# Performance work log

Measured on AMD Instinct MI355X. Metric: run time of the kernel, lower is better.

The kernel has to match this reference:

```python
import jax, jax.numpy as jnp
import numpy as np

# Config matching init_kwargs: dim=256, input_resolution=(64,64), num_heads=8,
# stride=2, dynamic_factor=2, window_size=8, Attention_Group=2, postype='rel', k=None
DIM, H, W = 256, 64, 64
HEADS, HG, STRIDE, WS, FACTOR = 8, 2, 2, 8, 2.0
GC = DIM // HG                 # channels per attention group (offset net width)
HC = DIM // HEADS              # per-head channels
RH, RW = H // STRIDE, W // STRIDE
WH, WW = H // WS, W // WS
B = 2
MLP_HID = 4 * DIM
EPS = 1e-5


def _grid_sample(img, grid):
    # img: (N, C, H, W); grid: (N, Hg, Wg, 2) with (row, col) in [-1, 1].
    # Bilinear, align_corners=True, zero padding (matches F.grid_sample).
    N, C, Hi, Wi = img.shape
    rows = (grid[..., 0] + 1.0) * 0.5 * (Hi - 1)
    cols = (grid[..., 1] + 1.0) * 0.5 * (Wi - 1)
    r0f = jnp.floor(rows); c0f = jnp.floor(cols)
    wr = rows - r0f; wc = cols - c0f
    r0 = r0f.astype(jnp.int32); c0 = c0f.astype(jnp.int32)

    def gather(ri, ci):
        valid = ((ri >= 0) & (ri < Hi) & (ci >= 0) & (ci < Wi)).astype(img.dtype)
        rc = jnp.clip(ri, 0, Hi - 1); cc = jnp.clip(ci, 0, Wi - 1)
        vals = jax.vmap(lambda im, r, c: im[:, r, c])(img, rc, cc)  # (N, C, Hg, Wg)
        return vals * valid[:, None]

    return (gather(r0, c0) * ((1 - wr) * (1 - wc))[:, None]
            + gather(r0, c0 + 1) * ((1 - wr) * wc)[:, None]
            + gather(r0 + 1, c0) * (wr * (1 - wc))[:, None]
            + gather(r0 + 1, c0 + 1) * (wr * wc)[:, None])


def _ln2d(z, g, b):
    mu = jnp.mean(z, axis=1, keepdims=True)
    var = jnp.var(z, axis=1, keepdims=True)
    return (z - mu) * jax.lax.rsqrt(var + EPS) * g[None, :, None, None] + b[None, :, None, None]


def _conv1x1(z, w, b=None):
    out = jnp.einsum('oc,bchw->bohw', w, z)
    return out if b is None else out + b[None, :, None, None]


def _forward(x, ln1_g, ln1_b, q_w, q_b, k_w, k_b, v_w, v_b,
             off1_w, off2_w, off3_w, bn_g, bn_b, bn_m, bn_v, off4_w,
             posembed, proj_w, proj_b, ln2_g, ln2_b,
             mlp_w1, mlp_b1, mlp_w2, mlp_b2):
    Bx, C = x.shape[0], x.shape[1]
    R, NW, WT = RH * RW, WH * WW, WS * WS
    scale = C ** -0.5  # original uses dim**-0.5 (not head_dim) as default qk scale

    xa = _ln2d(x, ln1_g, ln1_b)
    q = _conv1x1(xa, q_w, q_b)

    # ---- per-group offset prediction: 3 depthwise strided convs -> BN -> GELU -> 1x1 ----
    qg = q.reshape(Bx * HG, GC, H, W)

    def dw(z, w):
        return jax.lax.conv_general_dilated(z, w, (2, 2), ((1, 1), (1, 1)),
                feature_group_count=GC, dimension_numbers=('NCHW', 'OIHW', 'NCHW'))

    o = dw(dw(dw(qg, off1_w), off2_w), off3_w)  # (B*HG, GC, WH, WW)
    o = (o - bn_m[None, :, None, None]) * jax.lax.rsqrt(bn_v + EPS)[None, :, None, None]
    o = o * bn_g[None, :, None, None] + bn_b[None, :, None, None]
    o = jax.nn.gelu(o, approximate=False)
    off = jnp.einsum('oc,bchw->bohw', off4_w, o)               # (B*HG, 2R, WH, WW)
    off = off.reshape(Bx * HG, 2, R, NW).transpose(0, 3, 2, 1)  # (B*HG, NW, R, 2)
    ranges = jnp.array([1.0 / H, 1.0 / W], dtype=x.dtype)
    off = jnp.tanh(off) * ranges * FACTOR

    # ---- reference points normalized to [-1, 1] (align_corners=True convention) ----
    ref_r = (jnp.arange(RH, dtype=x.dtype) * STRIDE) / (H - 1) * 2.0 - 1.0
    ref_c = (jnp.arange(RW, dtype=x.dtype) * STRIDE) / (W - 1) * 2.0 - 1.0
    ref = jnp.stack(jnp.meshgrid(ref_r, ref_c, indexing='ij'), axis=-1).reshape(R, 2)
    grid = off + ref[None, None]                                # (B*HG, NW, R, 2)

    # ---- deformable gather of values at predicted sample locations ----
    value = xa.reshape(Bx * HG, GC, H, W)
    samp = _grid_sample(value, grid).reshape(Bx, C, NW, R)

    kk = _conv1x1(samp, k_w, k_b).reshape(Bx * HEADS, HC, NW, R).transpose(0, 2, 1, 3)
    vv = _conv1x1(samp, v_w, v_b).reshape(Bx * HEADS, HC, NW, R).transpose(0, 2, 1, 3)

    # ---- windowed queries ----
    wq = q.reshape(Bx * HEADS, HC, H, W).transpose(0, 2, 3, 1)
    wq = wq.reshape(Bx * HEADS, WH, WS, WW, WS, HC).transpose(0, 1, 3, 2, 4, 5)
    wq = wq.reshape(Bx * HEADS, NW, WT, HC) * scale

    attn = jnp.einsum('nwqc,nwcr->nwqr', wq, kk)                # (B*h, NW, WT, R)

    # ---- relative position bias: query pixel vs. (stride-spaced) reference point ----
    rel_y = (jnp.arange(RH) * STRIDE)[None, :] - jnp.arange(H)[:, None] + (H - 1)  # (H, RH)
    rel_x = (jnp.arange(RW) * STRIDE)[None, :] - jnp.arange(W)[:, None] + (W - 1)  # (W, RW)
    t = posembed[:, rel_y, :]                                   # (h, H, RH, 2W-1)
    bias = t[:, :, :, rel_x]                                    # (h, H, RH, W, RW)
    bias = bias.transpose(0, 1, 3, 2, 4).reshape(HEADS, H, W, R)
    bias = bias.reshape(HEADS, WH, WS, WW, WS, R).transpose(0, 1, 3, 2, 4, 5)
    bias = bias.reshape(HEADS, NW, WT, R)

    attn = attn.reshape(Bx, HEADS, NW, WT, R) + bias[None]
    attn = jax.nn.softmax(attn, axis=-1).reshape(Bx * HEADS, NW, WT, R)
    out = jnp.einsum('nwqr,nwcr->nwqc', attn, vv)               # (B*h, NW, WT, HC)
    out = out.reshape(Bx * HEADS, WH, WW, WS, WS, HC).transpose(0, 1, 3, 2, 4, 5)
    out = out.reshape(Bx, HEADS, H, W, HC).transpose(0, 1, 4, 2, 3).reshape(Bx, C, H, W)
    out = _conv1x1(out, proj_w, proj_b)

    x = x + out
    xm = _ln2d(x, ln2_g, ln2_b)
    hdn = jax.nn.gelu(_conv1x1(xm, mlp_w1, mlp_b1), approximate=False)
    return x + _conv1x1(hdn, mlp_w2, mlp_b2)


def setup_inputs() -> dict:
    key = jax.random.key(0)
    ks = jax.random.split(key, 16)
    f32 = jnp.float32

    def n(k, shape, std=0.02):
        return jax.random.normal(k, shape, dtype=f32) * std

    R = RH * RW
    return {
        'x': jax.random.normal(ks[0], (B, DIM, H, W), dtype=f32),
        'ln1_g': jnp.ones((DIM,), f32), 'ln1_b': jnp.zeros((DIM,), f32),
        'q_w': n(ks[1], (DIM, DIM)), 'q_b': jnp.zeros((DIM,), f32),
        'k_w': n(ks[2], (DIM, DIM)), 'k_b': jnp.zeros((DIM,), f32),
        'v_w': n(ks[3], (DIM, DIM)), 'v_b': jnp.zeros((DIM,), f32),
        'off1_w': n(ks[4], (GC, 1, 3, 3)),
        'off2_w': n(ks[5], (GC, 1, 3, 3)),
        'off3_w': n(ks[6], (GC, 1, 3, 3)),
        'bn_g': jnp.ones((GC,), f32), 'bn_b': jnp.zeros((GC,), f32),
        'bn_m': jnp.zeros((GC,), f32), 'bn_v': jnp.ones((GC,), f32),
        'off4_w': n(ks[7], (2 * R, GC)),
        'posembed': n(ks[8], (HEADS, 2 * H - 1, 2 * W - 1), std=0.01),
        'proj_w': n(ks[9], (DIM, DIM)), 'proj_b': jnp.zeros((DIM,), f32),
        'ln2_g': jnp.ones((DIM,), f32), 'ln2_b': jnp.zeros((DIM,), f32),
        'mlp_w1': n(ks[10], (MLP_HID, DIM)), 'mlp_b1': jnp.zeros((MLP_HID,), f32),
        'mlp_w2': n(ks[11], (DIM, MLP_HID)), 'mlp_b2': jnp.zeros((DIM,), f32),
    }


def reference(x, ln1_g, ln1_b, q_w, q_b, k_w, k_b, v_w, v_b,
              off1_w, off2_w, off3_w, bn_g, bn_b, bn_m, bn_v, off4_w,
              posembed, proj_w, proj_b, ln2_g, ln2_b,
              mlp_w1, mlp_b1, mlp_w2, mlp_b2):
    return _forward(x, ln1_g, ln1_b, q_w, q_b, k_w, k_b, v_w, v_b,
                    off1_w, off2_w, off3_w, bn_g, bn_b, bn_m, bn_v, off4_w,
                    posembed, proj_w, proj_b, ln2_g, ln2_b,
                    mlp_w1, mlp_b1, mlp_w2, mlp_b2)
```

## Files before the change

kernel.cpp:

```cpp
#include <hip/hip_runtime.h>
#include <hip/hip_bf16.h>
#include <math.h>


typedef __hip_bfloat16 bf16;
typedef __bf16 bf16x8 __attribute__((ext_vector_type(8)));
typedef float f32x4 __attribute__((ext_vector_type(4)));
typedef unsigned int u32x4 __attribute__((ext_vector_type(4)));

union U16x8 { uint4 u4; u32x4 v4; unsigned short us[8]; };

__device__ __forceinline__ float cvt(float x) { return x; }
__device__ __forceinline__ float cvt(bf16 x) { return __bfloat162float(x); }
__device__ __forceinline__ float b2f(unsigned short u) {
  union { float f; unsigned int v; } x; x.v = ((unsigned int)u) << 16; return x.f;
}
__device__ __forceinline__ unsigned short f2b(float f) {
  bf16 h = __float2bfloat16(f);
  return *reinterpret_cast<unsigned short*>(&h);
}
__device__ __forceinline__ float gelu_f(float x) {
  return 0.5f * x * (1.0f + erff(x * 0.7071067811865475f));
}
__device__ __forceinline__ void stout(float* p, float v) { *p = v; }
__device__ __forceinline__ void stout(bf16* p, float v) { *p = __float2bfloat16(v); }

__global__ __launch_bounds__(256) void setup_kernel(
    const float* __restrict__ x, const float* __restrict__ g,
    const float* __restrict__ bta,
    const float* __restrict__ q_w, const float* __restrict__ q_b,
    const float* __restrict__ k_w, const float* __restrict__ v_w,
    const float* __restrict__ pjw, const float* __restrict__ w1,
    const float* __restrict__ w2, const float* __restrict__ off4w,
    bf16* __restrict__ out, float* __restrict__ xnhwc,
    unsigned short* __restrict__ wqkv, float* __restrict__ bqkv,
    unsigned short* __restrict__ wproj, unsigned short* __restrict__ wmlp1,
    unsigned short* __restrict__ wmlp2, unsigned short* __restrict__ woff4i)
{
  __shared__ float s1[8][32], s2[8][32];
  __shared__ unsigned short tb[32][264];
  int bid = blockIdx.x;
  int t = threadIdx.x;
  if (bid < 256) {
    int pos = t & 31, cs = t >> 5;
    int p = bid * 32 + pos;
    int bb = p >> 12, hw = p & 4095;
    const float* xp = x + (size_t)bb * 256 * 4096 + hw;
    float vloc[32];
    float sum = 0.f, ss = 0.f;
#pragma unroll
    for (int i = 0; i < 32; ++i) {
      float v = xp[(size_t)(cs * 32 + i) * 4096];
      vloc[i] = v; sum += v; ss += v * v;
    }
    s1[cs][pos] = sum; s2[cs][pos] = ss;
    {
      float* xo = xnhwc + (size_t)p * 256 + cs * 32;
#pragma unroll
      for (int qd = 0; qd < 8; ++qd)
        *(float4*)(xo + qd * 4) = make_float4(vloc[qd*4], vloc[qd*4+1],
                                              vloc[qd*4+2], vloc[qd*4+3]);
    }
    __syncthreads();
    if (cs == 0) {
      float S = 0.f, Q = 0.f;
#pragma unroll
      for (int i = 0; i < 8; ++i) { S += s1[i][pos]; Q += s2[i][pos]; }
      float mu = S * (1.f / 256.f);
      float var = Q * (1.f / 256.f) - mu * mu;
      s1[0][pos] = mu;
      s2[0][pos] = rsqrtf(var + 1e-5f);
    }
    __syncthreads();
    float mu = s1[0][pos], rs = s2[0][pos];
#pragma unroll
    for (int i = 0; i < 32; ++i) {
      int c = cs * 32 + i;
      tb[pos][c] = f2b((vloc[i] - mu) * rs * g[c] + bta[c]);
    }
    __syncthreads();
    int px = t >> 3, grp = t & 7;
    bf16* op = out + ((size_t)bid * 32 + px) * 256 + grp * 32;
#pragma unroll
    for (int q = 0; q < 4; ++q)
      *(uint4*)(op + q * 8) = *(const uint4*)&tb[px][grp * 32 + q * 8];
  } else {
    int idx = (bid - 256) * 256 + t;
    const int S0 = 768 * 256;
    const int S1 = S0 + 768;
    const int S2 = S1 + 256 * 256;
    const int S3 = S2 + 1024 * 256;
    const int S4 = S3 + 256 * 1024;
    const int S5 = S4 + 2048 * 128;
    if (idx < S0) {
      int n = idx >> 8, c = idx & 255;
      float v;
      if (n < 256)       v = q_w[n * 256 + c];
      else if (n < 512)  v = k_w[(n - 256) * 256 + c];
      else               v = v_w[(n - 512) * 256 + c];
      wqkv[idx] = f2b(v);
    } else if (idx < S1) {
      int n = idx - S0;
      bqkv[n] = (n < 256) ? q_b[n] : 0.f;
    } else if (idx < S2) {
      wproj[idx - S1] = f2b(pjw[idx - S1]);
    } else if (idx < S3) {
      wmlp1[idx - S2] = f2b(w1[idx - S2]);
    } else if (idx < S4) {
      wmlp2[idx - S3] = f2b(w2[idx - S3]);
    } else if (idx < S5) {
      int kk = idx - S4;
      int n = kk >> 7, c = kk & 127;
      woff4i[kk] = f2b(off4w[((size_t)((n & 1) * 1024 + (n >> 1))) * 128 + c]);
    }
  }
}

__global__ __launch_bounds__(256) void ln2_kernel(
    const bf16* __restrict__ xin, const float* __restrict__ g,
    const float* __restrict__ bta, bf16* __restrict__ out)
{
  __shared__ float sa[8][32], sb[8][32];
  __shared__ float mu_s[32], rs_s[32];
  int t = threadIdx.x;
  int px = t >> 3, grp = t & 7;
  size_t p = (size_t)blockIdx.x * 32 + px;
  const bf16* xp = xin + p * 256 + grp * 32;
  float v[32]; float sum = 0.f, ss = 0.f;
#pragma unroll
  for (int q = 0; q < 4; ++q) {
    U16x8 u; u.u4 = *(const uint4*)(xp + q * 8);
#pragma unroll
    for (int j = 0; j < 8; ++j) {
      float f = b2f(u.us[j]); v[q * 8 + j] = f; sum += f; ss += f * f;
    }
  }
  sa[grp][px] = sum; sb[grp][px] = ss;
  __syncthreads();
  if (t < 32) {
    float S = 0.f, Q = 0.f;
#pragma unroll
    for (int i = 0; i < 8; ++i) { S += sa[i][t]; Q += sb[i][t]; }
    float mu = S * (1.f / 256.f);
    mu_s[t] = mu;
    rs_s[t] = rsqrtf(Q * (1.f / 256.f) - mu * mu + 1e-5f);
  }
  __syncthreads();
  float mu = mu_s[px], rs = rs_s[px];
  bf16* op = out + p * 256 + grp * 32;
#pragma unroll
  for (int q = 0; q < 4; ++q) {
    U16x8 o;
#pragma unroll
    for (int j = 0; j < 8; ++j) {
      int c = grp * 32 + q * 8 + j;
      o.us[j] = f2b((v[q * 8 + j] - mu) * rs * g[c] + bta[c]);
    }
    *(uint4*)(op + q * 8) = o.u4;
  }
}

template<int OUTM, int RESM, int ACT, int BM>
__global__ __launch_bounds__(256) void mgemm_kernel(
    const bf16* __restrict__ A, const unsigned short* __restrict__ Bw,
    const float* __restrict__ bias, const void* __restrict__ res,
    void* __restrict__ out, int N, int K, int lda, int ldb)
{
  constexpr int MT = BM / 32;
  constexpr int AB_BYTES = (BM + 64) * 72 * 2;
  constexpr int T_LD = BM + 5;
  constexpr int T_BYTES = 64 * T_LD * 4;
  constexpr int SH_BYTES = (OUTM == 1 && T_BYTES > AB_BYTES) ? T_BYTES : AB_BYTES;
  __shared__ __attribute__((aligned(16))) char shraw[SH_BYTES];
  auto As = reinterpret_cast<unsigned short(*)[72]>(shraw);
  auto Bs = reinterpret_cast<unsigned short(*)[72]>(shraw + BM * 72 * 2);
  float (*T)[T_LD] = reinterpret_cast<float(*)[T_LD]>(shraw);

  int t = threadIdx.x;
  int m0 = blockIdx.y * BM, n0 = blockIdx.x * 64;
  int lane = t & 63, w = t >> 6;
  int l15 = lane & 15, quad = lane >> 4;
  int wm = (w >> 1) * (BM / 2), wn = (w & 1) * 32;
  f32x4 acc[MT][2];
#pragma unroll
  for (int mt = 0; mt < MT; ++mt)
#pragma unroll
    for (int nt = 0; nt < 2; ++nt) acc[mt][nt] = (f32x4){0.f, 0.f, 0.f, 0.f};

  for (int k0 = 0; k0 < K; k0 += 64) {
#pragma unroll
    for (int i = 0; i < MT; ++i) {
      int idx = t + i * 256;
      int m = idx >> 3, oc = (idx & 7) * 8;
      *(uint4*)&As[m][oc] = *(const uint4*)(A + (size_t)(m0 + m) * lda + k0 + oc);
    }
#pragma unroll
    for (int i = 0; i < 2; ++i) {
      int idx = t + i * 256;
      int n = idx >> 3, oc = (idx & 7) * 8;
      *(uint4*)&Bs[n][oc] = *(const uint4*)(Bw + (size_t)(n0 + n) * ldb + k0 + oc);
    }
    __syncthreads();
#pragma unroll
    for (int ks = 0; ks < 2; ++ks) {
      bf16x8 af[MT], bfr[2];
#pragma unroll
      for (int mt = 0; mt < MT; ++mt)
        af[mt] = __builtin_bit_cast(bf16x8,
            *(const uint4*)&As[wm + mt * 16 + l15][ks * 32 + quad * 8]);
#pragma unroll
      for (int nt = 0; nt < 2; ++nt)
        bfr[nt] = __builtin_bit_cast(bf16x8,
            *(const uint4*)&Bs[wn + nt * 16 + l15][ks * 32 + quad * 8]);
#pragma unroll
      for (int mt = 0; mt < MT; ++mt)
#pragma unroll
        for (int nt = 0; nt < 2; ++nt)
          acc[mt][nt] = __builtin_amdgcn_mfma_f32_16x16x32_bf16(
              af[mt], bfr[nt], acc[mt][nt], 0, 0, 0);
    }
    __syncthreads();
  }
  float bv[2];
#pragma unroll
  for (int nt = 0; nt < 2; ++nt)
    bv[nt] = bias ? bias[n0 + wn + nt * 16 + l15] : 0.f;
#pragma unroll
  for (int mt = 0; mt < MT; ++mt) {
#pragma unroll
    for (int nt = 0; nt < 2; ++nt) {
#pragma unroll
      for (int reg = 0; reg < 4; ++reg) {
        int m = m0 + wm + mt * 16 + quad * 4 + reg;
        int n = n0 + wn + nt * 16 + l15;
        float v = acc[mt][nt][reg] + bv[nt];
        if constexpr (ACT == 1) v = gelu_f(v);
        if constexpr (RESM == 1)
          v += ((const float*)res)[(size_t)m * N + n];
        if constexpr (RESM == 2)
          v += b2f(((const unsigned short*)res)[(size_t)m * N + n]);
        if constexpr (OUTM == 0)
          ((unsigned short*)out)[(size_t)m * N + n] = f2b(v);
        if constexpr (OUTM == 1)
          T[(n - n0)][(m - m0)] = v;
        if constexpr (OUTM == 4)
          ((unsigned short*)out)[((size_t)(n >> 8) * 8192 + m) * 256 + (n & 255)] = f2b(v);
        if constexpr (OUTM == 5) {
          float val = tanhf(v) * (2.0f / 64.0f);
          int r = n >> 1, coord = n & 1;
          int rc = coord ? (r & 31) : (r >> 5);
          float ref = rc * (4.0f / 63.0f) - 1.0f;
          float pix = (val + ref + 1.0f) * 31.5f;
          float other = __shfl_xor(pix, 1, 64);
          if (coord == 0) {
            float rowp = pix, colp = other;
            float r0f = floorf(rowp), c0f = floorf(colp);
            float wr = rowp - r0f, wc = colp - c0f;
            int r0 = (int)r0f, c0 = (int)c0f;
            bool rv0 = ((unsigned)r0 < 64u), rv1 = ((unsigned)(r0 + 1) < 64u);
            bool cv0 = ((unsigned)c0 < 64u), cv1 = ((unsigned)(c0 + 1) < 64u);
            float4 w4;
            w4.x = (rv0 && cv0) ? (1.f - wr) * (1.f - wc) : 0.f;
            w4.y = (rv0 && cv1) ? (1.f - wr) * wc : 0.f;
            w4.z = (rv1 && cv0) ? wr * (1.f - wc) : 0.f;
            w4.w = (rv1 && cv1) ? wr * wc : 0.f;
            ((int*)out)[(size_t)m * 1024 + r] = r0 * 64 + c0;
            *(float4*)((float*)res + ((size_t)m * 1024 + r) * 4) = w4;
          }
        }
      }
    }
  }
  if constexpr (OUTM == 1) {
    __syncthreads();
    constexpr int SEGS = BM / 32;
    int units = 64 * SEGS;
    if (t < units) {
      int nl = t / SEGS, seg = t % SEGS;
      int bI = m0 >> 12, hw0 = m0 & 4095;
      float* op = (float*)out + ((size_t)bI * 256 + n0 + nl) * 4096 + hw0 + seg * 32;
#pragma unroll
      for (int k = 0; k < 32; ++k) op[k] = T[nl][seg * 32 + k];
    }
  }
}

template<typename TI, typename TO, int IC>
__global__ __launch_bounds__(256) void dwconv_kernel(
    const TI* __restrict__ in, const float* __restrict__ wgt,
    TO* __restrict__ out, int Hi, int Wi, int Ho, int Wo, int fuse,
    const float* __restrict__ bg_, const float* __restrict__ bb_,
    const float* __restrict__ bm_, const float* __restrict__ bv_)
{
  int idx = blockIdx.x * 256 + threadIdx.x;
  int c = idx & 127;
  int pp = idx >> 7;
  int ow = pp % Wo, oh = (pp / Wo) % Ho, bgi = pp / (Wo * Ho);
  const TI* ip;
  if constexpr (IC == 256)
    ip = in + ((size_t)(bgi >> 1) * 4096) * 256 + (bgi & 1) * 128 + c;
  else
    ip = in + ((size_t)bgi * Hi * Wi) * 128 + c;
  float acc = 0.f;
#pragma unroll
  for (int ky = 0; ky < 3; ++ky) {
    int ih = oh * 2 - 1 + ky;
    if ((unsigned)ih >= (unsigned)Hi) continue;
#pragma unroll
    for (int kx = 0; kx < 3; ++kx) {
      int iw = ow * 2 - 1 + kx;
      if ((unsigned)iw >= (unsigned)Wi) continue;
      acc += wgt[c * 9 + ky * 3 + kx] * cvt(ip[(size_t)(ih * Wi + iw) * IC]);
    }
  }
  if (fuse) {
    acc = (acc - bm_[c]) * rsqrtf(bv_[c] + 1e-5f) * bg_[c] + bb_[c];
    acc = gelu_f(acc);
  }
  stout(out + idx, acc);
}

__global__ __launch_bounds__(256) void gather1_kernel(
    const unsigned short* __restrict__ img,
    const int* __restrict__ goff, const float* __restrict__ gwt,
    unsigned short* __restrict__ outp)
{
  int blk = blockIdx.x;
  blk = (blk & 7) * 2048 + (blk >> 3);
  int t = threadIdx.x;
  int pos = blk * 8 + (t >> 5);
  int oct = t & 31;
  int r = pos & 1023;
  int nw = (pos >> 10) & 63;
  int b = pos >> 16;
  int ch0 = oct * 8;
  int g = oct >> 4;

  size_t cbase = ((size_t)(b * 2 + g) * 64 + nw) * 1024 + r;
  int base = goff[cbase];
  f32x4 wv = *(const f32x4*)(gwt + cbase * 4);
  int o00 = min(max(base, 0), 4095);
  int o01 = min(max(base + 1, 0), 4095);
  int o10 = min(max(base + 64, 0), 4095);
  int o11 = min(max(base + 65, 0), 4095);
  size_t pb = ((size_t)b * 4096) * 256 + ch0;
  uint4 cc[4];
  cc[0] = *(const uint4*)(img + pb + (size_t)o00 * 256);
  cc[1] = *(const uint4*)(img + pb + (size_t)o01 * 256);
  cc[2] = *(const uint4*)(img + pb + (size_t)o10 * 256);
  cc[3] = *(const uint4*)(img + pb + (size_t)o11 * 256);

  float a[8] = {0.f, 0.f, 0.f, 0.f, 0.f, 0.f, 0.f, 0.f};
#pragma unroll
  for (int c4 = 0; c4 < 4; ++c4) {
    U16x8 u; u.u4 = cc[c4];
    float wvv = wv[c4];
#pragma unroll
    for (int j = 0; j < 8; ++j) a[j] += wvv * b2f(u.us[j]);
  }
  U16x8 o;
#pragma unroll
  for (int j = 0; j < 8; ++j) o.us[j] = f2b(a[j]);
  int head = oct >> 2, chh = (oct & 3) * 8;
  size_t obase = (((size_t)(b * 8 + head) * 64 + nw) * 1024 + r) * 32 + chh;
  __builtin_nontemporal_store(o.v4, (u32x4*)(outp + obase));
}

__global__ __launch_bounds__(256) void attn2_kernel(
    const bf16* __restrict__ qbuf, const unsigned short* __restrict__ Ks,
    const unsigned short* __restrict__ Vs, const float* __restrict__ vbv,
    const float* __restrict__ pe, bf16* __restrict__ aout)
{
  __shared__ unsigned short vs[2][32][72];
  __shared__ unsigned short PsQs[64][72];
  __shared__ unsigned short pesb[70][72];

  int blk = blockIdx.x;
  int b = blk & 1, head = (blk >> 1) & 7, nw = blk >> 4;
  int wh = nw >> 3, ww = nw & 7;
  int t = threadIdx.x;
  int lane = t & 63, w = t >> 6;
  int l15 = lane & 15, quad = lane >> 4;
  int qc0 = head * 32;
  int vr = t >> 2, vseg = t & 3;

  size_t kvbase = ((size_t)(b * 8 + head) * 64 + nw) * 1024 * 32;
  const unsigned short* Kb = Ks + kvbase;
  const unsigned short* Vb = Vs + kvbase;

  {
    int qt = t >> 2, oct = t & 3;
    int h = wh * 8 + (qt >> 3), wcol = ww * 8 + (qt & 7);
    const bf16* src = qbuf + ((size_t)b * 4096 + h * 64 + wcol) * 256 + qc0 + oct * 8;
    U16x8 u; u.u4 = *(const uint4*)src;
    U16x8 o;
#pragma unroll
    for (int j = 0; j < 8; ++j) o.us[j] = f2b(b2f(u.us[j]) * 0.0625f);
    *(uint4*)&PsQs[qt][oct * 8] = o.u4;
  }
  int ry0 = 56 - wh * 8, rx0 = 56 - ww * 8;
  for (int i = t; i < 70 * 70; i += 256) {
    int yy = i / 70, xx = i % 70;
    pesb[yy][xx] = f2b(pe[(size_t)head * 16129 + (ry0 + yy) * 127 + rx0 + xx]);
  }
  {
    U16x8 vu; vu.u4 = *(const uint4*)(Vb + (size_t)t * 8);
#pragma unroll
    for (int j = 0; j < 8; ++j) {
      int row = vseg * 8 + j;
      vs[0][row][vr ^ (((row >> 3) & 3) * 8)] = vu.us[j];
    }
  }
  uint4 kf[4];
#pragma unroll
  for (int nt = 0; nt < 4; ++nt)
    kf[nt] = *(const uint4*)(Kb + (size_t)(nt * 16 + l15) * 32 + quad * 8);
  __syncthreads();

  bf16x8 aQ = __builtin_bit_cast(bf16x8, *(const uint4*)&PsQs[w * 16 + l15][quad * 8]);
  float l[4] = {0.f, 0.f, 0.f, 0.f};
  f32x4 oacc[2];
  oacc[0] = (f32x4){0.f, 0.f, 0.f, 0.f};
  oacc[1] = (f32x4){0.f, 0.f, 0.f, 0.f};

  uint4 vcn = make_uint4(0u, 0u, 0u, 0u);
  uint4 kfn[4];
  for (int c = 0; c < 16; ++c) {
    int cur = c & 1, rc0 = c * 64;
    if (c) {
      U16x8 vu; vu.u4 = vcn;
#pragma unroll
      for (int j = 0; j < 8; ++j) {
        int row = vseg * 8 + j;
        vs[cur][row][vr ^ (((row >> 3) & 3) * 8)] = vu.us[j];
      }
      __syncthreads();
    }
    if (c < 15) {
      size_t nb = (size_t)(rc0 + 64) * 32;
      vcn = *(const uint4*)(Vb + nb + (size_t)t * 8);
#pragma unroll
      for (int nt = 0; nt < 4; ++nt)
        kfn[nt] = *(const uint4*)(Kb + nb + (size_t)(nt * 16 + l15) * 32 + quad * 8);
    }

    f32x4 s[4];
#pragma unroll
    for (int nt = 0; nt < 4; ++nt) {
      bf16x8 bK = __builtin_bit_cast(bf16x8, kf[nt]);
      f32x4 z = (f32x4){0.f, 0.f, 0.f, 0.f};
      s[nt] = __builtin_amdgcn_mfma_f32_16x16x32_bf16(aQ, bK, z, 0, 0, 0);
    }
#pragma unroll
    for (int nt = 0; nt < 4; ++nt) {
      int rg_ = nt * 16 + l15;
      int rrow = (rc0 + rg_) >> 5, rcol = rg_ & 31;
#pragma unroll
      for (int reg = 0; reg < 4; ++reg) {
        int q = w * 16 + quad * 4 + reg;
        s[nt][reg] += b2f(pesb[2 * rrow + 7 - (q >> 3)][2 * rcol + 7 - (q & 7)]);
      }
    }
#pragma unroll
    for (int reg = 0; reg < 4; ++reg) {
      float ps = 0.f;
#pragma unroll
      for (int nt = 0; nt < 4; ++nt) {
        float p = __expf(s[nt][reg]);
        PsQs[w * 16 + quad * 4 + reg][nt * 16 + l15] = f2b(p);
        ps += p;
      }
      l[reg] += ps;
    }
#pragma unroll
    for (int kst = 0; kst < 2; ++kst) {
      uint4 up = *(const uint4*)&PsQs[w * 16 + l15][kst * 32 + quad * 8];
      bf16x8 pA = __builtin_bit_cast(bf16x8, up);
#pragma unroll
      for (int nt2 = 0; nt2 < 2; ++nt2) {
        int row = nt2 * 16 + l15;
        int cbase = (kst * 32 + quad * 8) ^ (((row >> 3) & 3) * 8);
        uint4 uv = *(const uint4*)&vs[cur][row][cbase];
        bf16x8 vB = __builtin_bit_cast(bf16x8, uv);
        oacc[nt2] = __builtin_amdgcn_mfma_f32_16x16x32_bf16(pA, vB, oacc[nt2], 0, 0, 0);
      }
    }
    if (c < 15) {
#pragma unroll
      for (int nt = 0; nt < 4; ++nt) kf[nt] = kfn[nt];
    }
  }
#pragma unroll
  for (int reg = 0; reg < 4; ++reg) {
    l[reg] += __shfl_xor(l[reg], 1, 64);
    l[reg] += __shfl_xor(l[reg], 2, 64);
    l[reg] += __shfl_xor(l[reg], 4, 64);
    l[reg] += __shfl_xor(l[reg], 8, 64);
  }
#pragma unroll
  for (int nt2 = 0; nt2 < 2; ++nt2) {
    float vbias = vbv[qc0 + nt2 * 16 + l15];
#pragma unroll
    for (int reg = 0; reg < 4; ++reg) {
      int q = w * 16 + quad * 4 + reg;
      size_t p = (size_t)b * 4096 + (wh * 8 + (q >> 3)) * 64 + ww * 8 + (q & 7);
      aout[p * 256 + qc0 + nt2 * 16 + l15] =
          __float2bfloat16(oacc[nt2][reg] / l[reg] + vbias);
    }
  }
}

extern "C" void kernel_launch(void* const* d_in, const int* in_sizes, int n_in,
                              void* d_out, int out_size, void* d_ws, size_t ws_size,
                              hipStream_t stream) {
  (void)in_sizes; (void)n_in; (void)out_size; (void)ws_size;
  const float* x     = (const float*)d_in[0];
  const float* ln1g  = (const float*)d_in[1];
  const float* ln1b  = (const float*)d_in[2];
  const float* q_w   = (const float*)d_in[3];
  const float* q_b   = (const float*)d_in[4];
  const float* k_w   = (const float*)d_in[5];
  const float* k_b   = (const float*)d_in[6];
  const float* v_w   = (const float*)d_in[7];
  const float* v_b   = (const float*)d_in[8];
  const float* off1w = (const float*)d_in[9];
  const float* off2w = (const float*)d_in[10];
  const float* off3w = (const float*)d_in[11];
  const float* bng   = (const float*)d_in[12];
  const float* bnb   = (const float*)d_in[13];
  const float* bnm   = (const float*)d_in[14];
  const float* bnv   = (const float*)d_in[15];
  const float* off4w = (const float*)d_in[16];
  const float* pe    = (const float*)d_in[17];
  const float* pjw   = (const float*)d_in[18];
  const float* pjb   = (const float*)d_in[19];
  const float* ln2g  = (const float*)d_in[20];
  const float* ln2b  = (const float*)d_in[21];
  const float* w1    = (const float*)d_in[22];
  const float* b1    = (const float*)d_in[23];
  const float* w2    = (const float*)d_in[24];
  const float* b2    = (const float*)d_in[25];
  (void)k_b;
  float* outp = (float*)d_out;

  char* W = (char*)d_ws;
  bf16*  xa    = (bf16*) (W + 0);
  float* dw1   = (float*)(W + 8388608);
  float* dw2   = (float*)(W + 10485760);
  bf16*  dw3b  = (bf16*) (W + 11010048);
  bf16*  qkv   = (bf16*) (W + 13238272);
  bf16*  qb    = qkv;
  bf16*  Kimg  = qkv + 2097152;
  bf16*  Vimg  = qkv + 2 * 2097152;
  bf16*  x2    = (bf16*) (W + 34209792);
  float* xnhwc = (float*)(W + 38404096);
  unsigned short* wqkv   = (unsigned short*)(W + 46792704);
  float*          bqkv   = (float*)         (W + 47448064);
  unsigned short* wproj  = (unsigned short*)(W + 47453184);
  unsigned short* wmlp1  = (unsigned short*)(W + 47584256);
  unsigned short* wmlp2  = (unsigned short*)(W + 48108544);
  unsigned short* woff4i = (unsigned short*)(W + 48632832);
  int*   goff  = (int*)  (W + 49157120);
  float* gwt   = (float*)(W + 50205696);
  unsigned short* Ksmp = (unsigned short*)(W + 54525952);
  unsigned short* Vsmp = (unsigned short*)(W + 121634816);
  bf16*  aout = xa;
  bf16*  xm   = xa;
  bf16*  hdn  = Kimg;

  setup_kernel<<<4356, 256, 0, stream>>>(
      x, ln1g, ln1b, q_w, q_b, k_w, v_w, pjw, w1, w2, off4w,
      xa, xnhwc, wqkv, bqkv, wproj, wmlp1, wmlp2, woff4i);
  mgemm_kernel<4, 0, 0, 128><<<dim3(12, 64), 256, 0, stream>>>(
      xa, wqkv, bqkv, nullptr, qkv, 768, 256, 256, 256);
  dwconv_kernel<bf16, float, 256><<<2048, 256, 0, stream>>>(
      qb, off1w, dw1, 64, 64, 32, 32, 0, nullptr, nullptr, nullptr, nullptr);
  dwconv_kernel<float, float, 128><<<512, 256, 0, stream>>>(
      dw1, off2w, dw2, 32, 32, 16, 16, 0, nullptr, nullptr, nullptr, nullptr);
  dwconv_kernel<float, bf16, 128><<<128, 256, 0, stream>>>(
      dw2, off3w, dw3b, 16, 16, 8, 8, 1, bng, bnb, bnm, bnv);
  mgemm_kernel<5, 0, 0, 128><<<dim3(32, 2), 256, 0, stream>>>(
      dw3b, woff4i, nullptr, (const void*)gwt, goff, 2048, 128, 128, 128);
  gather1_kernel<<<16384, 256, 0, stream>>>(
      (const unsigned short*)Kimg, goff, gwt, Ksmp);
  gather1_kernel<<<16384, 256, 0, stream>>>(
      (const unsigned short*)Vimg, goff, gwt, Vsmp);
  attn2_kernel<<<1024, 256, 0, stream>>>(
      qb, Ksmp, Vsmp, v_b, pe, aout);
  mgemm_kernel<0, 1, 0, 64><<<dim3(4, 128), 256, 0, stream>>>(
      aout, wproj, pjb, (const void*)xnhwc, x2, 256, 256, 256, 256);
  ln2_kernel<<<256, 256, 0, stream>>>(x2, ln2g, ln2b, xm);
  mgemm_kernel<0, 0, 1, 128><<<dim3(16, 64), 256, 0, stream>>>(
      xm, wmlp1, b1, nullptr, hdn, 1024, 256, 256, 256);
  mgemm_kernel<1, 2, 0, 64><<<dim3(4, 128), 256, 0, stream>>>(
      hdn, wmlp2, b2, (const void*)x2, outp, 256, 1024, 1024, 1024);
}
```

Baseline: 283.6 us.

## Gather V transposed and feed attention MFMA directly from registers

A new gather kernel writes sampled V in a channel-major (transposed) layout, so the attention kernel can load V B-operands straight from global memory into registers. This removes the per-chunk LDS transpose and its __syncthreads. The softmax also moves to exp2 by folding log2(e) into the Q scale and the position-embedding table. The positional-bias lookup is simplified to two 32-bit LDS reads per tile. In exchange, each thread in the gather kernel holds more registers (an 8x8 accumulator), and the V global loads in attention are strided by 1024 elements.

```diff
diff --git a/kernel.cpp b/kernel.cpp
--- a/kernel.cpp
+++ b/kernel.cpp
@@ -9,11 +9,18 @@
 typedef unsigned int u32x4 __attribute__((ext_vector_type(4)));
 
 union U16x8 { uint4 u4; u32x4 v4; unsigned short us[8]; };
+union FU { float f; unsigned int u; };
 
 __device__ __forceinline__ float cvt(float x) { return x; }
 __device__ __forceinline__ float cvt(bf16 x) { return __bfloat162float(x); }
 __device__ __forceinline__ float b2f(unsigned short u) {
   union { float f; unsigned int v; } x; x.v = ((unsigned int)u) << 16; return x.f;
+}
+__device__ __forceinline__ float hi2f(unsigned int u) {
+  FU x; x.u = u & 0xffff0000u; return x.f;
+}
+__device__ __forceinline__ float lo2f(unsigned int u) {
+  FU x; x.u = u << 16; return x.f;
 }
 __device__ __forceinline__ unsigned short f2b(float f) {
   bf16 h = __float2bfloat16(f);
@@ -366,15 +373,75 @@
   __builtin_nontemporal_store(o.v4, (u32x4*)(outp + obase));
 }
 
-__global__ __launch_bounds__(256) void attn2_kernel(
+__global__ __launch_bounds__(256) void gathert_kernel(
+    const unsigned short* __restrict__ img,
+    const int* __restrict__ goff, const float* __restrict__ gwt,
+    unsigned short* __restrict__ outp)
+{
+  int t = threadIdx.x;
+  int l = t & 63, wv_ = t >> 6;
+  int gw = blockIdx.x * 4 + wv_;
+  int win = gw >> 6;
+  int wq = gw & 63;
+  int ocb = wq & 3;
+  int r0 = (wq >> 2) * 64;
+  int b = win >> 6, nw = win & 63;
+  int lo3 = l & 7, hi3 = l >> 3;
+  int oc = ocb * 8 + hi3;
+  int ch0 = oc * 8;
+  int g = oc >> 4;
+  int rl = r0 + lo3 * 8;
+
+  size_t cb0 = ((size_t)(b * 2 + g) * 64 + nw) * 1024 + rl;
+  size_t pb = (size_t)b * 4096 * 256 + ch0;
+
+  float acc[8][8];
+#pragma unroll
+  for (int j = 0; j < 8; ++j)
+#pragma unroll
+    for (int i = 0; i < 8; ++i) acc[j][i] = 0.f;
+
+#pragma unroll
+  for (int i = 0; i < 8; ++i) {
+    int base = goff[cb0 + i];
+    f32x4 wv4 = *(const f32x4*)(gwt + (cb0 + i) * 4);
+    int o00 = min(max(base, 0), 4095);
+    int o01 = min(max(base + 1, 0), 4095);
+    int o10 = min(max(base + 64, 0), 4095);
+    int o11 = min(max(base + 65, 0), 4095);
+    uint4 cc[4];
+    cc[0] = *(const uint4*)(img + pb + (size_t)o00 * 256);
+    cc[1] = *(const uint4*)(img + pb + (size_t)o01 * 256);
+    cc[2] = *(const uint4*)(img + pb + (size_t)o10 * 256);
+    cc[3] = *(const uint4*)(img + pb + (size_t)o11 * 256);
+#pragma unroll
+    for (int c4 = 0; c4 < 4; ++c4) {
+      U16x8 u; u.u4 = cc[c4];
+      float wvv = wv4[c4];
+#pragma unroll
+      for (int j = 0; j < 8; ++j) acc[j][i] += wvv * b2f(u.us[j]);
+    }
+  }
+  int head = oc >> 2;
+  size_t rowb0 = (((size_t)(b * 8 + head) * 64 + nw) * 32 + (oc & 3) * 8);
+#pragma unroll
+  for (int j = 0; j < 8; ++j) {
+    U16x8 o;
+#pragma unroll
+    for (int k = 0; k < 8; ++k) o.us[k] = f2b(acc[j][k]);
+    __builtin_nontemporal_store(o.v4, (u32x4*)(outp + (rowb0 + j) * 1024 + rl));
+  }
+}
+
+__global__ __launch_bounds__(256) void attn3_kernel(
     const bf16* __restrict__ qbuf, const unsigned short* __restrict__ Ks,
-    const unsigned short* __restrict__ Vs, const float* __restrict__ vbv,
+    const unsigned short* __restrict__ Vts, const float* __restrict__ vbv,
     const float* __restrict__ pe, bf16* __restrict__ aout)
 {
-  __shared__ unsigned short vs[2][32][72];
   __shared__ unsigned short PsQs[64][72];
   __shared__ unsigned short pesb[70][72];
 
+  const float LOG2E = 1.4426950408889634f;
   int blk = blockIdx.x;
   int b = blk & 1, head = (blk >> 1) & 7, nw = blk >> 4;
   int wh = nw >> 3, ww = nw & 7;
@@ -382,11 +449,10 @@
   int lane = t & 63, w = t >> 6;
   int l15 = lane & 15, quad = lane >> 4;
   int qc0 = head * 32;
-  int vr = t >> 2, vseg = t & 3;
-
-  size_t kvbase = ((size_t)(b * 8 + head) * 64 + nw) * 1024 * 32;
+
+  size_t kvbase = ((size_t)(b * 8 + head) * 64 + nw) * 32768;
   const unsigned short* Kb = Ks + kvbase;
-  const unsigned short* Vb = Vs + kvbase;
+  const unsigned short* Vt = Vts + kvbase;
 
   {
     int qt = t >> 2, oct = t & 3;
@@ -395,26 +461,24 @@
     U16x8 u; u.u4 = *(const uint4*)src;
     U16x8 o;
 #pragma unroll
-    for (int j = 0; j < 8; ++j) o.us[j] = f2b(b2f(u.us[j]) * 0.0625f);
+    for (int j = 0; j < 8; ++j) o.us[j] = f2b(b2f(u.us[j]) * (0.0625f * LOG2E));
     *(uint4*)&PsQs[qt][oct * 8] = o.u4;
   }
   int ry0 = 56 - wh * 8, rx0 = 56 - ww * 8;
   for (int i = t; i < 70 * 70; i += 256) {
     int yy = i / 70, xx = i % 70;
-    pesb[yy][xx] = f2b(pe[(size_t)head * 16129 + (ry0 + yy) * 127 + rx0 + xx]);
-  }
-  {
-    U16x8 vu; vu.u4 = *(const uint4*)(Vb + (size_t)t * 8);
-#pragma unroll
-    for (int j = 0; j < 8; ++j) {
-      int row = vseg * 8 + j;
-      vs[0][row][vr ^ (((row >> 3) & 3) * 8)] = vu.us[j];
-    }
-  }
-  uint4 kf[4];
+    pesb[yy][xx] = f2b(pe[(size_t)head * 16129 + (ry0 + yy) * 127 + rx0 + xx] * LOG2E);
+  }
+  uint4 kf[4], vf[4];
 #pragma unroll
   for (int nt = 0; nt < 4; ++nt)
     kf[nt] = *(const uint4*)(Kb + (size_t)(nt * 16 + l15) * 32 + quad * 8);
+#pragma unroll
+  for (int kst = 0; kst < 2; ++kst)
+#pragma unroll
+    for (int nt2 = 0; nt2 < 2; ++nt2)
+      vf[kst * 2 + nt2] = *(const uint4*)(Vt + (size_t)(nt2 * 16 + l15) * 1024 +
+                                          kst * 32 + quad * 8);
   __syncthreads();
 
   bf16x8 aQ = __builtin_bit_cast(bf16x8, *(const uint4*)&PsQs[w * 16 + l15][quad * 8]);
@@ -423,25 +487,23 @@
   oacc[0] = (f32x4){0.f, 0.f, 0.f, 0.f};
   oacc[1] = (f32x4){0.f, 0.f, 0.f, 0.f};
 
-  uint4 vcn = make_uint4(0u, 0u, 0u, 0u);
-  uint4 kfn[4];
+  int rowbase = 7 - (w * 2 + (quad >> 1));
+  int Cb = 2 * l15 + 7 - (quad & 1) * 4;
+
+  uint4 kfn[4], vfn[4];
   for (int c = 0; c < 16; ++c) {
-    int cur = c & 1, rc0 = c * 64;
-    if (c) {
-      U16x8 vu; vu.u4 = vcn;
-#pragma unroll
-      for (int j = 0; j < 8; ++j) {
-        int row = vseg * 8 + j;
-        vs[cur][row][vr ^ (((row >> 3) & 3) * 8)] = vu.us[j];
-      }
-      __syncthreads();
-    }
+    int rc0 = c * 64;
     if (c < 15) {
-      size_t nb = (size_t)(rc0 + 64) * 32;
-      vcn = *(const uint4*)(Vb + nb + (size_t)t * 8);
+      int nb = rc0 + 64;
 #pragma unroll
       for (int nt = 0; nt < 4; ++nt)
-        kfn[nt] = *(const uint4*)(Kb + nb + (size_t)(nt * 16 + l15) * 32 + quad * 8);
+        kfn[nt] = *(const uint4*)(Kb + (size_t)(nb + nt * 16 + l15) * 32 + quad * 8);
+#pragma unroll
+      for (int kst = 0; kst < 2; ++kst)
+#pragma unroll
+        for (int nt2 = 0; nt2 < 2; ++nt2)
+          vfn[kst * 2 + nt2] = *(const uint4*)(Vt + (size_t)(nt2 * 16 + l15) * 1024 +
+                                               nb + kst * 32 + quad * 8);
     }
 
     f32x4 s[4];
@@ -453,20 +515,22 @@
     }
 #pragma unroll
     for (int nt = 0; nt < 4; ++nt) {
-      int rg_ = nt * 16 + l15;
-      int rrow = (rc0 + rg_) >> 5, rcol = rg_ & 31;
-#pragma unroll
-      for (int reg = 0; reg < 4; ++reg) {
-        int q = w * 16 + quad * 4 + reg;
-        s[nt][reg] += b2f(pesb[2 * rrow + 7 - (q >> 3)][2 * rcol + 7 - (q & 7)]);
-      }
+      int row = rowbase + 4 * c + 2 * (nt >> 1);
+      int C = Cb + (nt & 1) * 32;
+      const unsigned int* pr = (const unsigned int*)&pesb[row][0];
+      unsigned int pa = pr[(C - 3) >> 1];
+      unsigned int pbm = pr[(C - 1) >> 1];
+      s[nt][0] += hi2f(pbm);
+      s[nt][1] += lo2f(pbm);
+      s[nt][2] += hi2f(pa);
+      s[nt][3] += lo2f(pa);
     }
 #pragma unroll
     for (int reg = 0; reg < 4; ++reg) {
       float ps = 0.f;
 #pragma unroll
       for (int nt = 0; nt < 4; ++nt) {
-        float p = __expf(s[nt][reg]);
+        float p = exp2f(s[nt][reg]);
         PsQs[w * 16 + quad * 4 + reg][nt * 16 + l15] = f2b(p);
         ps += p;
       }
@@ -478,16 +542,13 @@
       bf16x8 pA = __builtin_bit_cast(bf16x8, up);
 #pragma unroll
       for (int nt2 = 0; nt2 < 2; ++nt2) {
-        int row = nt2 * 16 + l15;
-        int cbase = (kst * 32 + quad * 8) ^ (((row >> 3) & 3) * 8);
-        uint4 uv = *(const uint4*)&vs[cur][row][cbase];
-        bf16x8 vB = __builtin_bit_cast(bf16x8, uv);
+        bf16x8 vB = __builtin_bit_cast(bf16x8, vf[kst * 2 + nt2]);
         oacc[nt2] = __builtin_amdgcn_mfma_f32_16x16x32_bf16(pA, vB, oacc[nt2], 0, 0, 0);
       }
     }
     if (c < 15) {
 #pragma unroll
-      for (int nt = 0; nt < 4; ++nt) kf[nt] = kfn[nt];
+      for (int i = 0; i < 4; ++i) { kf[i] = kfn[i]; vf[i] = vfn[i]; }
     }
   }
 #pragma unroll
@@ -563,7 +624,7 @@
   int*   goff  = (int*)  (W + 49157120);
   float* gwt   = (float*)(W + 50205696);
   unsigned short* Ksmp = (unsigned short*)(W + 54525952);
-  unsigned short* Vsmp = (unsigned short*)(W + 121634816);
+  unsigned short* Vts  = (unsigned short*)(W + 121634816);
   bf16*  aout = xa;
   bf16*  xm   = xa;
   bf16*  hdn  = Kimg;
@@ -583,10 +644,10 @@
       dw3b, woff4i, nullptr, (const void*)gwt, goff, 2048, 128, 128, 128);
   gather1_kernel<<<16384, 256, 0, stream>>>(
       (const unsigned short*)Kimg, goff, gwt, Ksmp);
-  gather1_kernel<<<16384, 256, 0, stream>>>(
-      (const unsigned short*)Vimg, goff, gwt, Vsmp);
-  attn2_kernel<<<1024, 256, 0, stream>>>(
-      qb, Ksmp, Vsmp, v_b, pe, aout);
+  gathert_kernel<<<2048, 256, 0, stream>>>(
+      (const unsigned short*)Vimg, goff, gwt, Vts);
+  attn3_kernel<<<1024, 256, 0, stream>>>(
+      qb, Ksmp, Vts, v_b, pe, aout);
   mgemm_kernel<0, 1, 0, 64><<<dim3(4, 128), 256, 0, stream>>>(
       aout, wproj, pjb, (const void*)xnhwc, x2, 256, 256, 256, 256);
   ln2_kernel<<<256, 256, 0, stream>>>(x2, ln2g, ln2b, xm);
```

After: 319.5 us. +12.7%, slower.

## Split attention over key halves with a merge kernel; use exp2

Applied to the files above, without the earlier changes.

The attention kernel now splits each window's 1024 sampled keys into two halves processed by separate blocks, giving 2048 blocks instead of 1024. Each block writes unnormalized fp32 partial outputs and row sums, and a new merge kernel adds the halves, normalizes and adds the value bias. Because there is no running max, the two partial sums combine by plain addition. Scores are prescaled by log2(e) so exp2f can replace __expf. The split costs extra fp32 partial-output traffic and one more launch, and it falls back to the unsplit kernel if the workspace is too small.

```diff
diff --git a/kernel.cpp b/kernel.cpp
--- a/kernel.cpp
+++ b/kernel.cpp
@@ -366,16 +366,24 @@
   __builtin_nontemporal_store(o.v4, (u32x4*)(outp + obase));
 }
 
-__global__ __launch_bounds__(256) void attn2_kernel(
+template<int NH>
+__global__ __launch_bounds__(256) void attn2s_kernel(
     const bf16* __restrict__ qbuf, const unsigned short* __restrict__ Ks,
     const unsigned short* __restrict__ Vs, const float* __restrict__ vbv,
-    const float* __restrict__ pe, bf16* __restrict__ aout)
+    const float* __restrict__ pe, bf16* __restrict__ aout,
+    float* __restrict__ Opart, float* __restrict__ lpart)
 {
+  constexpr int STAGES = 16 / NH;
+  constexpr int PESB_R = (NH == 1) ? 70 : 39;
   __shared__ unsigned short vs[2][32][72];
   __shared__ unsigned short PsQs[64][72];
-  __shared__ unsigned short pesb[70][72];
-
-  int blk = blockIdx.x;
+  __shared__ unsigned short pesb[PESB_R][72];
+
+  const float LOG2E = 1.4426950408889634f;
+  int blk0 = blockIdx.x;
+  int blk = blk0 & 1023;
+  int half = (NH == 2) ? (blk0 >> 10) : 0;
+  int rbase = half * (1024 / NH);
   int b = blk & 1, head = (blk >> 1) & 7, nw = blk >> 4;
   int wh = nw >> 3, ww = nw & 7;
   int t = threadIdx.x;
@@ -384,9 +392,9 @@
   int qc0 = head * 32;
   int vr = t >> 2, vseg = t & 3;
 
-  size_t kvbase = ((size_t)(b * 8 + head) * 64 + nw) * 1024 * 32;
-  const unsigned short* Kb = Ks + kvbase;
-  const unsigned short* Vb = Vs + kvbase;
+  size_t kvbase = ((size_t)(b * 8 + head) * 64 + nw) * 32768;
+  const unsigned short* Kb = Ks + kvbase + (size_t)rbase * 32;
+  const unsigned short* Vb = Vs + kvbase + (size_t)rbase * 32;
 
   {
     int qt = t >> 2, oct = t & 3;
@@ -395,13 +403,13 @@
     U16x8 u; u.u4 = *(const uint4*)src;
     U16x8 o;
 #pragma unroll
-    for (int j = 0; j < 8; ++j) o.us[j] = f2b(b2f(u.us[j]) * 0.0625f);
+    for (int j = 0; j < 8; ++j) o.us[j] = f2b(b2f(u.us[j]) * (0.0625f * LOG2E));
     *(uint4*)&PsQs[qt][oct * 8] = o.u4;
   }
-  int ry0 = 56 - wh * 8, rx0 = 56 - ww * 8;
-  for (int i = t; i < 70 * 70; i += 256) {
+  int ry0 = 56 - wh * 8 + 32 * half, rx0 = 56 - ww * 8;
+  for (int i = t; i < PESB_R * 70; i += 256) {
     int yy = i / 70, xx = i % 70;
-    pesb[yy][xx] = f2b(pe[(size_t)head * 16129 + (ry0 + yy) * 127 + rx0 + xx]);
+    pesb[yy][xx] = f2b(pe[(size_t)head * 16129 + (ry0 + yy) * 127 + rx0 + xx] * LOG2E);
   }
   {
     U16x8 vu; vu.u4 = *(const uint4*)(Vb + (size_t)t * 8);
@@ -425,7 +433,7 @@
 
   uint4 vcn = make_uint4(0u, 0u, 0u, 0u);
   uint4 kfn[4];
-  for (int c = 0; c < 16; ++c) {
+  for (int c = 0; c < STAGES; ++c) {
     int cur = c & 1, rc0 = c * 64;
     if (c) {
       U16x8 vu; vu.u4 = vcn;
@@ -436,7 +444,7 @@
       }
       __syncthreads();
     }
-    if (c < 15) {
+    if (c < STAGES - 1) {
       size_t nb = (size_t)(rc0 + 64) * 32;
       vcn = *(const uint4*)(Vb + nb + (size_t)t * 8);
 #pragma unroll
@@ -466,7 +474,7 @@
       float ps = 0.f;
 #pragma unroll
       for (int nt = 0; nt < 4; ++nt) {
-        float p = __expf(s[nt][reg]);
+        float p = exp2f(s[nt][reg]);
         PsQs[w * 16 + quad * 4 + reg][nt * 16 + l15] = f2b(p);
         ps += p;
       }
@@ -485,7 +493,7 @@
         oacc[nt2] = __builtin_amdgcn_mfma_f32_16x16x32_bf16(pA, vB, oacc[nt2], 0, 0, 0);
       }
     }
-    if (c < 15) {
+    if (c < STAGES - 1) {
 #pragma unroll
       for (int nt = 0; nt < 4; ++nt) kf[nt] = kfn[nt];
     }
@@ -497,23 +505,59 @@
     l[reg] += __shfl_xor(l[reg], 4, 64);
     l[reg] += __shfl_xor(l[reg], 8, 64);
   }
-#pragma unroll
-  for (int nt2 = 0; nt2 < 2; ++nt2) {
-    float vbias = vbv[qc0 + nt2 * 16 + l15];
-#pragma unroll
-    for (int reg = 0; reg < 4; ++reg) {
-      int q = w * 16 + quad * 4 + reg;
-      size_t p = (size_t)b * 4096 + (wh * 8 + (q >> 3)) * 64 + ww * 8 + (q & 7);
-      aout[p * 256 + qc0 + nt2 * 16 + l15] =
-          __float2bfloat16(oacc[nt2][reg] / l[reg] + vbias);
-    }
-  }
+  if constexpr (NH == 1) {
+#pragma unroll
+    for (int nt2 = 0; nt2 < 2; ++nt2) {
+      float vbias = vbv[qc0 + nt2 * 16 + l15];
+#pragma unroll
+      for (int reg = 0; reg < 4; ++reg) {
+        int q = w * 16 + quad * 4 + reg;
+        size_t p = (size_t)b * 4096 + (wh * 8 + (q >> 3)) * 64 + ww * 8 + (q & 7);
+        aout[p * 256 + qc0 + nt2 * 16 + l15] =
+            __float2bfloat16(oacc[nt2][reg] / l[reg] + vbias);
+      }
+    }
+  } else {
+    size_t ob = ((size_t)(half << 10 | blk)) * 2048;
+#pragma unroll
+    for (int nt2 = 0; nt2 < 2; ++nt2) {
+#pragma unroll
+      for (int reg = 0; reg < 4; ++reg) {
+        int q = w * 16 + quad * 4 + reg;
+        Opart[ob + q * 32 + nt2 * 16 + l15] = oacc[nt2][reg];
+      }
+    }
+    if (l15 == 0) {
+      size_t lb = ((size_t)(half << 10 | blk)) * 64;
+#pragma unroll
+      for (int reg = 0; reg < 4; ++reg)
+        lpart[lb + w * 16 + quad * 4 + reg] = l[reg];
+    }
+  }
+}
+
+__global__ __launch_bounds__(256) void attnmerge_kernel(
+    const float* __restrict__ Opart, const float* __restrict__ lpart,
+    const float* __restrict__ vbv, bf16* __restrict__ aout)
+{
+  int t = threadIdx.x;
+  int widx = blockIdx.x * 8 + (t >> 5);
+  int ch = t & 31;
+  int win = widx >> 6, q = widx & 63;
+  int b = win & 1, head = (win >> 1) & 7, nw = win >> 4;
+  int wh = nw >> 3, ww = nw & 7;
+  size_t o0 = (size_t)win * 2048 + q * 32 + ch;
+  float O = Opart[o0] + Opart[(size_t)(1 << 10) * 2048 + o0];
+  float L = lpart[(size_t)win * 64 + q] + lpart[(size_t)(1024 + win) * 64 + q];
+  float vbias = vbv[head * 32 + ch];
+  size_t p = (size_t)b * 4096 + (wh * 8 + (q >> 3)) * 64 + ww * 8 + (q & 7);
+  aout[p * 256 + head * 32 + ch] = __float2bfloat16(O / L + vbias);
 }
 
 extern "C" void kernel_launch(void* const* d_in, const int* in_sizes, int n_in,
                               void* d_out, int out_size, void* d_ws, size_t ws_size,
                               hipStream_t stream) {
-  (void)in_sizes; (void)n_in; (void)out_size; (void)ws_size;
+  (void)in_sizes; (void)n_in; (void)out_size;
   const float* x     = (const float*)d_in[0];
   const float* ln1g  = (const float*)d_in[1];
   const float* ln1b  = (const float*)d_in[2];
@@ -564,6 +608,9 @@
   float* gwt   = (float*)(W + 50205696);
   unsigned short* Ksmp = (unsigned short*)(W + 54525952);
   unsigned short* Vsmp = (unsigned short*)(W + 121634816);
+  float* Opart = (float*)(W + 188743680);
+  float* lpart = (float*)(W + 205520896);
+  const size_t WS_NEED = 206045184ull;
   bf16*  aout = xa;
   bf16*  xm   = xa;
   bf16*  hdn  = Kimg;
@@ -585,8 +632,14 @@
       (const unsigned short*)Kimg, goff, gwt, Ksmp);
   gather1_kernel<<<16384, 256, 0, stream>>>(
       (const unsigned short*)Vimg, goff, gwt, Vsmp);
-  attn2_kernel<<<1024, 256, 0, stream>>>(
-      qb, Ksmp, Vsmp, v_b, pe, aout);
+  if (ws_size >= WS_NEED) {
+    attn2s_kernel<2><<<2048, 256, 0, stream>>>(
+        qb, Ksmp, Vsmp, v_b, pe, aout, Opart, lpart);
+    attnmerge_kernel<<<8192, 256, 0, stream>>>(Opart, lpart, v_b, aout);
+  } else {
+    attn2s_kernel<1><<<1024, 256, 0, stream>>>(
+        qb, Ksmp, Vsmp, v_b, pe, aout, nullptr, nullptr);
+  }
   mgemm_kernel<0, 1, 0, 64><<<dim3(4, 128), 256, 0, stream>>>(
       aout, wproj, pjb, (const void*)xnhwc, x2, 256, 256, 256, 256);
   ln2_kernel<<<256, 256, 0, stream>>>(x2, ln2g, ln2b, xm);
```

After: 295.8 us. 1.04x slower.
